# Performance work log

Hardware: AMD Instinct MI355X
Metric: run time of the kernel (lower is better)

Reference implementation:

```python
import jax, jax.numpy as jnp
import numpy as np

D_MODEL = 1024
N_HEADS = 16
D_K = D_MODEL // N_HEADS


def setup_inputs() -> dict:
    key = jax.random.key(0)
    ks = jax.random.split(key, 10)
    B, L = 2, 2048
    s = 1.0 / np.sqrt(D_MODEL)
    inp = {
        "x": jax.random.normal(ks[0], (B, L, D_MODEL), dtype=jnp.float32),
        "bond_influence": jax.random.uniform(ks[1], (B, L, L), dtype=jnp.float32),
        "Wq": jax.random.uniform(ks[2], (D_MODEL, D_MODEL), jnp.float32, -s, s),
        "bq": jax.random.uniform(ks[3], (D_MODEL,), jnp.float32, -s, s),
        "Wk": jax.random.uniform(ks[4], (D_MODEL, D_MODEL), jnp.float32, -s, s),
        "bk": jax.random.uniform(ks[5], (D_MODEL,), jnp.float32, -s, s),
        "Wv": jax.random.uniform(ks[6], (D_MODEL, D_MODEL), jnp.float32, -s, s),
        "bv": jax.random.uniform(ks[7], (D_MODEL,), jnp.float32, -s, s),
        "Wo": jax.random.uniform(ks[8], (D_MODEL, D_MODEL), jnp.float32, -s, s),
        "bo": jax.random.uniform(ks[9], (D_MODEL,), jnp.float32, -s, s),
    }
    return inp


def reference(x, bond_influence, Wq, bq, Wk, bk, Wv, bv, Wo, bo):
    B, L, _ = x.shape
    # QKV projections -> [B, H, L, d_k]
    def proj(W, b):
        return (x @ W + b).reshape(B, L, N_HEADS, D_K).transpose(0, 2, 1, 3)
    Q = proj(Wq, bq)
    K = proj(Wk, bk)
    V = proj(Wv, bv)
    # scores: [B, H, L, L], scaled then modulated by per-batch bond influence
    scores = jnp.einsum('bhqd,bhkd->bhqk', Q, K) / jnp.sqrt(jnp.float32(D_K))
    scores = scores * bond_influence[:, None, :, :]
    attn = jax.nn.softmax(scores, axis=-1)
    out = jnp.einsum('bhqk,bhkd->bhqd', attn, V)  # [B, H, L, d_k]
    out = out.transpose(0, 2, 1, 3).reshape(B, L, D_MODEL)
    return out @ Wo + bo
```

## Files before the change

kernel.cpp:

```cpp
#include <hip/hip_runtime.h>
#include <stdint.h>

typedef unsigned short u16;
typedef __attribute__((ext_vector_type(8))) short bf16x8;
typedef __attribute__((ext_vector_type(4))) float f32x4;

__device__ __forceinline__ u16 f2bf(float f) {
    union { float f; uint32_t u; } v; v.f = f;
    uint32_t u = v.u + 0x7fffu + ((v.u >> 16) & 1u);
    return (u16)(u >> 16);
}
__device__ __forceinline__ float vexp2(float x) {
    float d;
    asm("v_exp_f32 %0, %1" : "=v"(d) : "v"(x));
    return d;
}
__device__ __forceinline__ uint32_t cvtpk(float a, float b) {
    uint32_t d;
    asm("v_cvt_pk_bf16_f32 %0, %1, %2" : "=v"(d) : "v"(a), "v"(b));
    return d;
}

__device__ __forceinline__ void gld16(const void* g, void* l) {
    __builtin_amdgcn_global_load_lds((const __attribute__((address_space(1))) void*)g,
                                     (__attribute__((address_space(3))) void*)l,
                                     16, 0, 0);
}

__device__ __forceinline__ void plswap16(uint32_t& a, uint32_t& b) {
    asm volatile("v_permlane16_swap_b32 %0, %1" : "+v"(a), "+v"(b));
}


__global__ void pack5_kernel(const float* __restrict__ Wq, const float* __restrict__ Wk,
                             const float* __restrict__ Wv, const float* __restrict__ Wo,
                             const float* __restrict__ x,
                             u16* __restrict__ dqkv, u16* __restrict__ dwo,
                             u16* __restrict__ dx) {
    const int z = blockIdx.z;
    const int tx = threadIdx.x, ty = threadIdx.y;
    if (z == 4) {
        const int bid = blockIdx.y * 32 + blockIdx.x;
        const int tid = ty * 32 + tx;
#pragma unroll
        for (int i = 0; i < 4; ++i) {
            const int idx = bid * 1024 + i * 256 + tid;
            float4 v = ((const float4*)x)[idx];
            ushort4 o;
            o.x = f2bf(v.x); o.y = f2bf(v.y); o.z = f2bf(v.z); o.w = f2bf(v.w);
            ((ushort4*)dx)[idx] = o;
        }
        return;
    }
    __shared__ float tile[32][33];
    const float* src = (z == 0) ? Wq : (z == 1) ? Wk : (z == 2) ? Wv : Wo;
    u16* dst = (z < 3) ? (dqkv + (size_t)z * 1024 * 1024) : dwo;
    const int bx = blockIdx.x * 32, by = blockIdx.y * 32;
#pragma unroll
    for (int i = ty; i < 32; i += 8)
        tile[i][tx] = src[(size_t)(by + i) * 1024 + bx + tx];
    __syncthreads();
#pragma unroll
    for (int i = ty; i < 32; i += 8)
        dst[(size_t)(bx + i) * 1024 + by + tx] = f2bf(tile[tx][i]);
}


template <int EPI>
__global__ __launch_bounds__(256) void gemm128(
    const u16* __restrict__ A, const u16* __restrict__ Bt,
    const float* __restrict__ bias0, const float* __restrict__ bias1,
    const float* __restrict__ bias2,
    u16* __restrict__ o_q, u16* __restrict__ o_k, u16* __restrict__ o_vt,
    float* __restrict__ o_f, int nbx)
{
    constexpr int K = 1024;
    __shared__ u16 As[128 * 64];
    __shared__ u16 Bs[128 * 64];
    const int t = threadIdx.x;
    const int lane = t & 63, w = t >> 6;
    const int wm = w >> 1, wn = w & 1;
    const int g = lane >> 4, r = lane & 15;
    const int sw = r & 7;
    const int f = blockIdx.x;
    const int cpx = (gridDim.x >> 3);
    const int swz = (f & 7) * cpx + (f >> 3);
    const int mbase = (swz / nbx) * 128, nbase = (swz % nbx) * 128;

    const f32x4 zero4 = {0.f, 0.f, 0.f, 0.f};
    f32x4 acc[4][4];
#pragma unroll
    for (int m = 0; m < 4; ++m)
#pragma unroll
        for (int n = 0; n < 4; ++n) acc[m][n] = zero4;

    for (int k0 = 0; k0 < K; k0 += 64) {
#pragma unroll
        for (int i = 0; i < 4; ++i) {
            const int idx = i * 256 + t;
            const int row = idx >> 3, ch = idx & 7;
            const int chg = ch ^ (row & 7);
            gld16(A + (size_t)(mbase + row) * K + k0 + chg * 8, (char*)As + idx * 16);
            gld16(Bt + (size_t)(nbase + row) * K + k0 + chg * 8, (char*)Bs + idx * 16);
        }
        __syncthreads();

#pragma unroll
        for (int kk = 0; kk < 2; ++kk) {
            bf16x8 af[4], bfr[4];
#pragma unroll
            for (int m = 0; m < 4; ++m) {
                const int row = wm * 64 + m * 16 + r;
                af[m] = *(const bf16x8*)((const char*)As + row * 128 + (((kk * 4 + g) ^ sw) << 4));
            }
#pragma unroll
            for (int n = 0; n < 4; ++n) {
                const int row = wn * 64 + n * 16 + r;
                bfr[n] = *(const bf16x8*)((const char*)Bs + row * 128 + (((kk * 4 + g) ^ sw) << 4));
            }
            __builtin_amdgcn_s_setprio(1);
#pragma unroll
            for (int m = 0; m < 4; ++m)
#pragma unroll
                for (int n = 0; n < 4; ++n)
                    acc[m][n] = __builtin_amdgcn_mfma_f32_16x16x32_bf16(af[m], bfr[n], acc[m][n], 0, 0, 0);
            __builtin_amdgcn_s_setprio(0);
        }
        __syncthreads();
    }

#pragma unroll
    for (int m = 0; m < 4; ++m) {
#pragma unroll
        for (int n = 0; n < 4; ++n) {
            const int c = nbase + wn * 64 + n * 16 + r;
#pragma unroll
            for (int j = 0; j < 4; ++j) {
                const int rr = mbase + wm * 64 + m * 16 + g * 4 + j;
                const float y = acc[m][n][j];
                if (EPI == 0) {
                    const int which = c >> 10, d = c & 1023;
                    const int b = rr >> 11, l = rr & 2047;
                    const int h = d >> 6, dd = d & 63;
                    const size_t bh = (size_t)(b * 16 + h);
                    if (which == 0) {
                        o_q[(bh * 2048 + l) * 64 + dd] = f2bf((y + bias0[d]) * 0.18033688011112042f);
                    } else if (which == 1) {
                        o_k[(bh * 2048 + l) * 64 + dd] = f2bf(y + bias1[d]);
                    } else {
                        o_vt[(bh * 64 + dd) * 2048 + l] = f2bf(y + bias2[d]);
                    }
                } else {
                    o_f[(size_t)rr * 1024 + c] = y + bias0[c];
                }
            }
        }
    }
}


#define ATTN_STEP(CUR, BD, BDN, PREF, WAITN)                                                 \
    {                                                                                        \
        if (PREF) {                                                                          \
            const int kt2 = kt + 64;                                                         \
            _Pragma("unroll")                                                                \
            for (int i = 0; i < 4; ++i) {                                                    \
                const int idx = i * 128 + t;                                                 \
                const int row = idx >> 3, ch = idx & 7;                                      \
                const int chg = ch ^ (row & 7);                                              \
                gld16(kb + kvBase + (size_t)(kt2 + row) * 64 + chg * 8,                      \
                      (char*)&Ks[CUR ^ 1][0] + idx * 16);                                    \
                gld16(vtb + vtBase + (size_t)row * 2048 + kt2 + chg * 8,                     \
                      (char*)&Vs[CUR ^ 1][0] + idx * 16);                                    \
            }                                                                                \
            _Pragma("unroll")                                                                \
            for (int qf = 0; qf < 2; ++qf)                                                   \
                _Pragma("unroll")                                                            \
                for (int kf = 0; kf < 4; ++kf)                                               \
                    BDN[qf][kf] = *(const float4*)&bondf[bondRow0 + (size_t)qf * 32768 +     \
                                                         kt2 + kf * 16 + g * 4];             \
        }                                                                                    \
        asm volatile("s_waitcnt vmcnt(" #WAITN ")" ::: "memory");                            \
        __builtin_amdgcn_s_barrier();                                                        \
        __builtin_amdgcn_sched_barrier(0);                                                   \
                                                                            \
        f32x4 st[2][4];                                                                      \
        {                                                                                    \
            bf16x8 kfr[2][2];                                                                \
            _Pragma("unroll")                                                                \
            for (int kz = 0; kz < 2; ++kz)                                                   \
                _Pragma("unroll")                                                            \
                for (int kf = 0; kf < 2; ++kf)                                               \
                    kfr[kz][kf] = *(const bf16x8*)((const char*)&Ks[CUR][0] +                \
                                    (kf * 16 + r) * 128 + (((kz * 4 + g) ^ sw) * 16));       \
            _Pragma("unroll")                                                                \
            for (int qf = 0; qf < 2; ++qf)                                                   \
                _Pragma("unroll")                                                            \
                for (int kf = 0; kf < 2; ++kf) st[qf][kf] = zero4;                           \
            __builtin_amdgcn_s_setprio(1);                                                   \
            _Pragma("unroll")                                                                \
            for (int kz = 0; kz < 2; ++kz)                                                   \
                _Pragma("unroll")                                                            \
                for (int qf = 0; qf < 2; ++qf)                                               \
                    _Pragma("unroll")                                                        \
                    for (int kf = 0; kf < 2; ++kf)                                           \
                        st[qf][kf] = __builtin_amdgcn_mfma_f32_16x16x32_bf16(                \
                            kfr[kz][kf], aq[qf][kz], st[qf][kf], 0, 0, 0);                   \
            __builtin_amdgcn_s_setprio(0);                                                   \
        }                                                                                    \
                                                                      \
        bf16x8 ap0[2], ap1[2];                                                               \
        _Pragma("unroll")                                                                    \
        for (int qf = 0; qf < 2; ++qf) {                                                     \
            uint32_t pkl[2], pkh[2];                                                         \
            _Pragma("unroll")                                                                \
            for (int kf = 0; kf < 2; ++kf) {                                                 \
                const float p0 = vexp2(st[qf][kf][0] * BD[qf][kf].x);                        \
                const float p1 = vexp2(st[qf][kf][1] * BD[qf][kf].y);                        \
                const float p2 = vexp2(st[qf][kf][2] * BD[qf][kf].z);                        \
                const float p3 = vexp2(st[qf][kf][3] * BD[qf][kf].w);                        \
                sm[qf] += (p0 + p1) + (p2 + p3);                                             \
                pkl[kf] = cvtpk(p0, p1);                                                     \
                pkh[kf] = cvtpk(p2, p3);                                                     \
            }                                                                                \
            plswap16(pkl[0], pkl[1]);                                                        \
            plswap16(pkh[0], pkh[1]);                                                        \
            union { uint32_t u[4]; bf16x8 v; } a_;                                           \
            a_.u[0] = pkl[0]; a_.u[1] = pkh[0]; a_.u[2] = pkl[1]; a_.u[3] = pkh[1];          \
            ap0[qf] = a_.v;                                                                  \
        }                                                                                    \
                                                                            \
        {                                                                                    \
            bf16x8 kfr[2][2];                                                                \
            _Pragma("unroll")                                                                \
            for (int kz = 0; kz < 2; ++kz)                                                   \
                _Pragma("unroll")                                                            \
                for (int kf = 0; kf < 2; ++kf)                                               \
                    kfr[kz][kf] = *(const bf16x8*)((const char*)&Ks[CUR][0] +                \
                                    ((kf + 2) * 16 + r) * 128 + (((kz * 4 + g) ^ sw) * 16)); \
            _Pragma("unroll")                                                                \
            for (int qf = 0; qf < 2; ++qf)                                                   \
                _Pragma("unroll")                                                            \
                for (int kf = 0; kf < 2; ++kf) st[qf][kf + 2] = zero4;                       \
            __builtin_amdgcn_s_setprio(1);                                                   \
            _Pragma("unroll")                                                                \
            for (int kz = 0; kz < 2; ++kz)                                                   \
                _Pragma("unroll")                                                            \
                for (int qf = 0; qf < 2; ++qf)                                               \
                    _Pragma("unroll")                                                        \
                    for (int kf = 0; kf < 2; ++kf)                                           \
                        st[qf][kf + 2] = __builtin_amdgcn_mfma_f32_16x16x32_bf16(            \
                            kfr[kz][kf], aq[qf][kz], st[qf][kf + 2], 0, 0, 0);               \
            __builtin_amdgcn_s_setprio(0);                                                   \
        }                                                                                    \
                                                                                \
        {                                                                                    \
            bf16x8 bv_[4];                                                                   \
            _Pragma("unroll")                                                                \
            for (int nf = 0; nf < 4; ++nf)                                                   \
                bv_[nf] = *(const bf16x8*)((const char*)&Vs[CUR][0] +                        \
                            (nf * 16 + r) * 128 + ((pg ^ sw) * 16));                         \
            __builtin_amdgcn_s_setprio(1);                                                   \
            _Pragma("unroll")                                                                \
            for (int qf = 0; qf < 2; ++qf)                                                   \
                _Pragma("unroll")                                                            \
                for (int nf = 0; nf < 4; ++nf)                                               \
                    o[qf][nf] = __builtin_amdgcn_mfma_f32_16x16x32_bf16(                     \
                        ap0[qf], bv_[nf], o[qf][nf], 0, 0, 0);                               \
            __builtin_amdgcn_s_setprio(0);                                                   \
        }                                                                                    \
                                                                      \
        _Pragma("unroll")                                                                    \
        for (int qf = 0; qf < 2; ++qf) {                                                     \
            uint32_t pkl[2], pkh[2];                                                         \
            _Pragma("unroll")                                                                \
            for (int kf = 0; kf < 2; ++kf) {                                                 \
                const float p0 = vexp2(st[qf][kf + 2][0] * BD[qf][kf + 2].x);                \
                const float p1 = vexp2(st[qf][kf + 2][1] * BD[qf][kf + 2].y);                \
                const float p2 = vexp2(st[qf][kf + 2][2] * BD[qf][kf + 2].z);                \
                const float p3 = vexp2(st[qf][kf + 2][3] * BD[qf][kf + 2].w);                \
                sm[qf] += (p0 + p1) + (p2 + p3);                                             \
                pkl[kf] = cvtpk(p0, p1);                                                     \
                pkh[kf] = cvtpk(p2, p3);                                                     \
            }                                                                                \
            plswap16(pkl[0], pkl[1]);                                                        \
            plswap16(pkh[0], pkh[1]);                                                        \
            union { uint32_t u[4]; bf16x8 v; } a_;                                           \
            a_.u[0] = pkl[0]; a_.u[1] = pkh[0]; a_.u[2] = pkl[1]; a_.u[3] = pkh[1];          \
            ap1[qf] = a_.v;                                                                  \
        }                                                                                    \
                                                                                \
        {                                                                                    \
            bf16x8 bv_[4];                                                                   \
            _Pragma("unroll")                                                                \
            for (int nf = 0; nf < 4; ++nf)                                                   \
                bv_[nf] = *(const bf16x8*)((const char*)&Vs[CUR][0] +                        \
                            (nf * 16 + r) * 128 + (((4 + pg) ^ sw) * 16));                   \
            __builtin_amdgcn_s_setprio(1);                                                   \
            _Pragma("unroll")                                                                \
            for (int qf = 0; qf < 2; ++qf)                                                   \
                _Pragma("unroll")                                                            \
                for (int nf = 0; nf < 4; ++nf)                                               \
                    o[qf][nf] = __builtin_amdgcn_mfma_f32_16x16x32_bf16(                     \
                        ap1[qf], bv_[nf], o[qf][nf], 0, 0, 0);                               \
            __builtin_amdgcn_s_setprio(0);                                                   \
        }                                                                                    \
        __builtin_amdgcn_sched_barrier(0);                                                   \
        __builtin_amdgcn_s_barrier();                                                        \
        kt += 64;                                                                            \
    }

__global__ __launch_bounds__(128, 2) void attn_kernel(
    const u16* __restrict__ qb, const u16* __restrict__ kb,
    const u16* __restrict__ vtb, const float* __restrict__ bondf,
    u16* __restrict__ attnout)
{
    __shared__ u16 Ks[2][64 * 64];
    __shared__ u16 Vs[2][64 * 64];
    const int t = threadIdx.x;
    const int lane = t & 63, w = t >> 6;
    const int g = lane >> 4, r = lane & 15;
    const int sw = r & 7;
    const int pg = ((g & 1) << 1) | (g >> 1);
    const int flat = blockIdx.x;
    const int x = flat & 7;
    const int j = flat >> 3;
    const int b = x >> 2;
    const int qt = (x & 3) * 8 + (j & 7);
    const int h = j >> 3;
    const int bh = b * 16 + h;
    const int q0 = qt * 64 + w * 32;
    const size_t kvBase = (size_t)bh * 2048 * 64;
    const size_t vtBase = (size_t)bh * 64 * 2048;
    const size_t bondRow0 = ((size_t)b * 2048 + q0 + r) * 2048;

    bf16x8 aq[2][2];
#pragma unroll
    for (int qf = 0; qf < 2; ++qf)
#pragma unroll
        for (int kz = 0; kz < 2; ++kz)
            aq[qf][kz] = *(const bf16x8*)&qb[kvBase + (size_t)(q0 + qf * 16 + r) * 64 + kz * 32 + g * 8];

    const f32x4 zero4 = {0.f, 0.f, 0.f, 0.f};
    f32x4 o[2][4];
#pragma unroll
    for (int qf = 0; qf < 2; ++qf)
#pragma unroll
        for (int nf = 0; nf < 4; ++nf) o[qf][nf] = zero4;
    float sm[2] = {0.f, 0.f};

#pragma unroll
    for (int i = 0; i < 4; ++i) {
        const int idx = i * 128 + t;
        const int row = idx >> 3, ch = idx & 7;
        const int chg = ch ^ (row & 7);
        gld16(kb + kvBase + (size_t)row * 64 + chg * 8, (char*)&Ks[0][0] + idx * 16);
        gld16(vtb + vtBase + (size_t)row * 2048 + chg * 8, (char*)&Vs[0][0] + idx * 16);
    }
    float4 bdA[2][4], bdB[2][4];
#pragma unroll
    for (int qf = 0; qf < 2; ++qf)
#pragma unroll
        for (int kf = 0; kf < 4; ++kf)
            bdA[qf][kf] = *(const float4*)&bondf[bondRow0 + (size_t)qf * 32768 + kf * 16 + g * 4];

    int kt = 0;
    for (int s = 0; s < 15; ++s) {
        ATTN_STEP(0, bdA, bdB, 1, 16)
        ATTN_STEP(1, bdB, bdA, 1, 16)
    }
    ATTN_STEP(0, bdA, bdB, 1, 16)
    ATTN_STEP(1, bdB, bdA, 0, 0)

#pragma unroll
    for (int qf = 0; qf < 2; ++qf) {
        sm[qf] += __shfl_xor(sm[qf], 16, 64);
        sm[qf] += __shfl_xor(sm[qf], 32, 64);
    }
#pragma unroll
    for (int qf = 0; qf < 2; ++qf)
#pragma unroll
        for (int j2 = 0; j2 < 4; ++j2) {
            const float inv = 1.f / __shfl(sm[qf], g * 4 + j2, 16);
            const size_t orow = ((size_t)b * 2048 + q0 + qf * 16 + g * 4 + j2) * 1024 + h * 64;
#pragma unroll
            for (int nf = 0; nf < 4; ++nf)
                attnout[orow + nf * 16 + r] = f2bf(o[qf][nf][j2] * inv);
        }
}


extern "C" void kernel_launch(void* const* d_in, const int* in_sizes, int n_in,
                              void* d_out, int out_size, void* d_ws, size_t ws_size,
                              hipStream_t stream) {
    (void)in_sizes; (void)n_in; (void)out_size; (void)ws_size;
    const float* x    = (const float*)d_in[0];
    const float* bond = (const float*)d_in[1];
    const float* Wq   = (const float*)d_in[2];
    const float* bq   = (const float*)d_in[3];
    const float* Wk   = (const float*)d_in[4];
    const float* bk   = (const float*)d_in[5];
    const float* Wv   = (const float*)d_in[6];
    const float* bv   = (const float*)d_in[7];
    const float* Wo   = (const float*)d_in[8];
    const float* bo   = (const float*)d_in[9];
    float* out = (float*)d_out;

    char* ws = (char*)d_ws;
    u16* xb      = (u16*)(ws);
    u16* wqkvt   = (u16*)(ws + 8388608);
    u16* wot     = (u16*)(ws + 14680064);
    u16* qb      = (u16*)(ws + 16777216);
    u16* kb_     = (u16*)(ws + 25165824);
    u16* vtb     = (u16*)(ws + 33554432);
    u16* attnout = (u16*)(ws + 58720256);

    pack5_kernel<<<dim3(32, 32, 5), dim3(32, 8), 0, stream>>>(Wq, Wk, Wv, Wo, x, wqkvt, wot, xb);

    gemm128<0><<<dim3(768), 256, 0, stream>>>(xb, wqkvt, bq, bk, bv, qb, kb_, vtb, nullptr, 24);
    attn_kernel<<<dim3(1024), 128, 0, stream>>>(qb, kb_, vtb, bond, attnout);
    gemm128<1><<<dim3(256), 256, 0, stream>>>(attnout, wot, bo, nullptr, nullptr,
                                              nullptr, nullptr, nullptr, out, 8);
}
```

Before: 153.5 us.

## Double-buffer GEMM LDS tiles to overlap global loads with MFMA compute

```diff
diff --git a/kernel.cpp b/kernel.cpp
--- a/kernel.cpp
+++ b/kernel.cpp
@@ -66,6 +66,47 @@
 }
 
 
+#define GEMM_STEP(CUR, K0N, PREF, WAITN)                                              \
+    {                                                                                 \
+        if (PREF) {                                                                   \
+            _Pragma("unroll")                                                         \
+            for (int i = 0; i < 4; ++i) {                                             \
+                const int idx = i * 256 + t;                                          \
+                const int row = idx >> 3, ch = idx & 7;                               \
+                const int chg = ch ^ (row & 7);                                       \
+                gld16(A + (size_t)(mbase + row) * 1024 + (K0N) + chg * 8,             \
+                      (char*)&As[CUR ^ 1][0] + idx * 16);                             \
+                gld16(Bt + (size_t)(nbase + row) * 1024 + (K0N) + chg * 8,            \
+                      (char*)&Bs[CUR ^ 1][0] + idx * 16);                             \
+            }                                                                         \
+        }                                                                             \
+        asm volatile("s_waitcnt vmcnt(" #WAITN ")" ::: "memory");                     \
+        __builtin_amdgcn_s_barrier();                                                 \
+        __builtin_amdgcn_sched_barrier(0);                                            \
+        _Pragma("unroll")                                                             \
+        for (int kk = 0; kk < 2; ++kk) {                                              \
+            bf16x8 af[4], bfr[4];                                                     \
+            _Pragma("unroll")                                                         \
+            for (int m = 0; m < 4; ++m)                                               \
+                af[m] = *(const bf16x8*)((const char*)&As[CUR][0] +                   \
+                        (wm * 64 + m * 16 + r) * 128 + (((kk * 4 + g) ^ sw) << 4));   \
+            _Pragma("unroll")                                                         \
+            for (int n = 0; n < 4; ++n)                                               \
+                bfr[n] = *(const bf16x8*)((const char*)&Bs[CUR][0] +                  \
+                        (wn * 64 + n * 16 + r) * 128 + (((kk * 4 + g) ^ sw) << 4));   \
+            __builtin_amdgcn_s_setprio(1);                                            \
+            _Pragma("unroll")                                                         \
+            for (int m = 0; m < 4; ++m)                                               \
+                _Pragma("unroll")                                                     \
+                for (int n = 0; n < 4; ++n)                                           \
+                    acc[m][n] = __builtin_amdgcn_mfma_f32_16x16x32_bf16(              \
+                        af[m], bfr[n], acc[m][n], 0, 0, 0);                           \
+            __builtin_amdgcn_s_setprio(0);                                            \
+        }                                                                             \
+        __builtin_amdgcn_sched_barrier(0);                                            \
+        __builtin_amdgcn_s_barrier();                                                 \
+    }
+
 template <int EPI>
 __global__ __launch_bounds__(256) void gemm128(
     const u16* __restrict__ A, const u16* __restrict__ Bt,
@@ -74,9 +115,8 @@
     u16* __restrict__ o_q, u16* __restrict__ o_k, u16* __restrict__ o_vt,
     float* __restrict__ o_f, int nbx)
 {
-    constexpr int K = 1024;
-    __shared__ u16 As[128 * 64];
-    __shared__ u16 Bs[128 * 64];
+    __shared__ u16 As[2][128 * 64];
+    __shared__ u16 Bs[2][128 * 64];
     const int t = threadIdx.x;
     const int lane = t & 63, w = t >> 6;
     const int wm = w >> 1, wn = w & 1;
@@ -94,40 +134,22 @@
 #pragma unroll
         for (int n = 0; n < 4; ++n) acc[m][n] = zero4;
 
-    for (int k0 = 0; k0 < K; k0 += 64) {
-#pragma unroll
-        for (int i = 0; i < 4; ++i) {
-            const int idx = i * 256 + t;
-            const int row = idx >> 3, ch = idx & 7;
-            const int chg = ch ^ (row & 7);
-            gld16(A + (size_t)(mbase + row) * K + k0 + chg * 8, (char*)As + idx * 16);
-            gld16(Bt + (size_t)(nbase + row) * K + k0 + chg * 8, (char*)Bs + idx * 16);
-        }
-        __syncthreads();
-
-#pragma unroll
-        for (int kk = 0; kk < 2; ++kk) {
-            bf16x8 af[4], bfr[4];
-#pragma unroll
-            for (int m = 0; m < 4; ++m) {
-                const int row = wm * 64 + m * 16 + r;
-                af[m] = *(const bf16x8*)((const char*)As + row * 128 + (((kk * 4 + g) ^ sw) << 4));
-            }
-#pragma unroll
-            for (int n = 0; n < 4; ++n) {
-                const int row = wn * 64 + n * 16 + r;
-                bfr[n] = *(const bf16x8*)((const char*)Bs + row * 128 + (((kk * 4 + g) ^ sw) << 4));
-            }
-            __builtin_amdgcn_s_setprio(1);
-#pragma unroll
-            for (int m = 0; m < 4; ++m)
-#pragma unroll
-                for (int n = 0; n < 4; ++n)
-                    acc[m][n] = __builtin_amdgcn_mfma_f32_16x16x32_bf16(af[m], bfr[n], acc[m][n], 0, 0, 0);
-            __builtin_amdgcn_s_setprio(0);
-        }
-        __syncthreads();
-    }
+#pragma unroll
+    for (int i = 0; i < 4; ++i) {
+        const int idx = i * 256 + t;
+        const int row = idx >> 3, ch = idx & 7;
+        const int chg = ch ^ (row & 7);
+        gld16(A + (size_t)(mbase + row) * 1024 + chg * 8, (char*)&As[0][0] + idx * 16);
+        gld16(Bt + (size_t)(nbase + row) * 1024 + chg * 8, (char*)&Bs[0][0] + idx * 16);
+    }
+
+    int k0 = 0;
+    for (int s = 0; s < 7; ++s) {
+        GEMM_STEP(0, k0 + 64, 1, 8) k0 += 64;
+        GEMM_STEP(1, k0 + 64, 1, 8) k0 += 64;
+    }
+    GEMM_STEP(0, k0 + 64, 1, 8) k0 += 64;
+    GEMM_STEP(1, 0, 0, 0)
 
 #pragma unroll
     for (int m = 0; m < 4; ++m) {
```

Measured after the change: 176.3 us. +14.9%, slower.

## Split attention over two key halves and merge partials in a combine kernel

Applied to the files above, without the earlier changes.

```diff
diff --git a/kernel.cpp b/kernel.cpp
--- a/kernel.cpp
+++ b/kernel.cpp
@@ -9,6 +9,10 @@
     union { float f; uint32_t u; } v; v.f = f;
     uint32_t u = v.u + 0x7fffu + ((v.u >> 16) & 1u);
     return (u16)(u >> 16);
+}
+__device__ __forceinline__ float bf2f(u16 s) {
+    union { uint32_t u; float f; } v; v.u = ((uint32_t)s) << 16;
+    return v.f;
 }
 __device__ __forceinline__ float vexp2(float x) {
     float d;
@@ -313,7 +317,7 @@
 __global__ __launch_bounds__(128, 2) void attn_kernel(
     const u16* __restrict__ qb, const u16* __restrict__ kb,
     const u16* __restrict__ vtb, const float* __restrict__ bondf,
-    u16* __restrict__ attnout)
+    u16* __restrict__ po, float* __restrict__ psm)
 {
     __shared__ u16 Ks[2][64 * 64];
     __shared__ u16 Vs[2][64 * 64];
@@ -324,12 +328,14 @@
     const int pg = ((g & 1) << 1) | (g >> 1);
     const int flat = blockIdx.x;
     const int x = flat & 7;
-    const int j = flat >> 3;
+    const int jj = flat >> 3;
     const int b = x >> 2;
-    const int qt = (x & 3) * 8 + (j & 7);
-    const int h = j >> 3;
+    const int qt = (x & 3) * 8 + (jj & 7);
+    const int h = (jj >> 3) & 15;
+    const int half = jj >> 7;
     const int bh = b * 16 + h;
     const int q0 = qt * 64 + w * 32;
+    const int kt0 = half * 1024;
     const size_t kvBase = (size_t)bh * 2048 * 64;
     const size_t vtBase = (size_t)bh * 64 * 2048;
     const size_t bondRow0 = ((size_t)b * 2048 + q0 + r) * 2048;
@@ -354,18 +360,18 @@
         const int idx = i * 128 + t;
         const int row = idx >> 3, ch = idx & 7;
         const int chg = ch ^ (row & 7);
-        gld16(kb + kvBase + (size_t)row * 64 + chg * 8, (char*)&Ks[0][0] + idx * 16);
-        gld16(vtb + vtBase + (size_t)row * 2048 + chg * 8, (char*)&Vs[0][0] + idx * 16);
+        gld16(kb + kvBase + (size_t)(kt0 + row) * 64 + chg * 8, (char*)&Ks[0][0] + idx * 16);
+        gld16(vtb + vtBase + (size_t)row * 2048 + kt0 + chg * 8, (char*)&Vs[0][0] + idx * 16);
     }
     float4 bdA[2][4], bdB[2][4];
 #pragma unroll
     for (int qf = 0; qf < 2; ++qf)
 #pragma unroll
         for (int kf = 0; kf < 4; ++kf)
-            bdA[qf][kf] = *(const float4*)&bondf[bondRow0 + (size_t)qf * 32768 + kf * 16 + g * 4];
-
-    int kt = 0;
-    for (int s = 0; s < 15; ++s) {
+            bdA[qf][kf] = *(const float4*)&bondf[bondRow0 + (size_t)qf * 32768 + kt0 + kf * 16 + g * 4];
+
+    int kt = kt0;
+    for (int s = 0; s < 7; ++s) {
         ATTN_STEP(0, bdA, bdB, 1, 16)
         ATTN_STEP(1, bdB, bdA, 1, 16)
     }
@@ -377,16 +383,58 @@
         sm[qf] += __shfl_xor(sm[qf], 16, 64);
         sm[qf] += __shfl_xor(sm[qf], 32, 64);
     }
-#pragma unroll
-    for (int qf = 0; qf < 2; ++qf)
+
+    const size_t unit2 = (size_t)(bh * 32 + qt) * 2 + half;
+    const size_t pbase = unit2 * 4096;
+#pragma unroll
+    for (int qf = 0; qf < 2; ++qf) {
+        if (g == 0) psm[unit2 * 64 + w * 32 + qf * 16 + r] = sm[qf];
 #pragma unroll
         for (int j2 = 0; j2 < 4; ++j2) {
-            const float inv = 1.f / __shfl(sm[qf], g * 4 + j2, 16);
-            const size_t orow = ((size_t)b * 2048 + q0 + qf * 16 + g * 4 + j2) * 1024 + h * 64;
+            const size_t prow = pbase + (size_t)(w * 32 + qf * 16 + g * 4 + j2) * 64;
 #pragma unroll
             for (int nf = 0; nf < 4; ++nf)
-                attnout[orow + nf * 16 + r] = f2bf(o[qf][nf][j2] * inv);
+                po[prow + nf * 16 + r] = f2bf(o[qf][nf][j2]);
         }
+    }
+}
+
+
+__global__ __launch_bounds__(256) void combine_kernel(
+    const u16* __restrict__ po, const float* __restrict__ psm,
+    u16* __restrict__ attnout)
+{
+    const int tt = blockIdx.x * 256 + threadIdx.x;
+    const size_t e = (size_t)tt * 8;
+    const int unit = (int)(e >> 12);
+    const int within = (int)(e & 4095);
+    const int row = within >> 6;
+    const int col = within & 63;
+    const int bh = unit >> 5, qt = unit & 31;
+    const int b = bh >> 4, h = bh & 15;
+
+    const size_t p0 = ((size_t)unit * 2) * 4096 + within;
+    const size_t p1 = p0 + 4096;
+    ushort4 a0 = *(const ushort4*)&po[p0];
+    ushort4 a1 = *(const ushort4*)&po[p0 + 4];
+    ushort4 b0 = *(const ushort4*)&po[p1];
+    ushort4 b1 = *(const ushort4*)&po[p1 + 4];
+    const float s0 = psm[((size_t)unit * 2) * 64 + row];
+    const float s1 = psm[((size_t)unit * 2 + 1) * 64 + row];
+    const float inv = 1.f / (s0 + s1);
+
+    const size_t orow = ((size_t)b * 2048 + qt * 64 + row) * 1024 + h * 64 + col;
+    ushort4 o0, o1;
+    o0.x = f2bf((bf2f(a0.x) + bf2f(b0.x)) * inv);
+    o0.y = f2bf((bf2f(a0.y) + bf2f(b0.y)) * inv);
+    o0.z = f2bf((bf2f(a0.z) + bf2f(b0.z)) * inv);
+    o0.w = f2bf((bf2f(a0.w) + bf2f(b0.w)) * inv);
+    o1.x = f2bf((bf2f(a1.x) + bf2f(b1.x)) * inv);
+    o1.y = f2bf((bf2f(a1.y) + bf2f(b1.y)) * inv);
+    o1.z = f2bf((bf2f(a1.z) + bf2f(b1.z)) * inv);
+    o1.w = f2bf((bf2f(a1.w) + bf2f(b1.w)) * inv);
+    *(ushort4*)&attnout[orow] = o0;
+    *(ushort4*)&attnout[orow + 4] = o1;
 }
 
 
@@ -413,12 +461,15 @@
     u16* qb      = (u16*)(ws + 16777216);
     u16* kb_     = (u16*)(ws + 25165824);
     u16* vtb     = (u16*)(ws + 33554432);
+    u16* po      = (u16*)(ws + 41943040);
+    float* psm   = (float*)(ws);
     u16* attnout = (u16*)(ws + 58720256);
 
     pack5_kernel<<<dim3(32, 32, 5), dim3(32, 8), 0, stream>>>(Wq, Wk, Wv, Wo, x, wqkvt, wot, xb);
 
     gemm128<0><<<dim3(768), 256, 0, stream>>>(xb, wqkvt, bq, bk, bv, qb, kb_, vtb, nullptr, 24);
-    attn_kernel<<<dim3(1024), 128, 0, stream>>>(qb, kb_, vtb, bond, attnout);
+    attn_kernel<<<dim3(2048), 128, 0, stream>>>(qb, kb_, vtb, bond, po, psm);
+    combine_kernel<<<dim3(2048), 256, 0, stream>>>(po, psm, attnout);
     gemm128<1><<<dim3(256), 256, 0, stream>>>(attnout, wot, bo, nullptr, nullptr,
                                               nullptr, nullptr, nullptr, out, 8);
 }
```

After: 165.8 us. +8.0%, slower.
